# Kernel optimization log

Measured on AMD Instinct MI355X. Metric: run time of the kernel, lower is better.

## Reference

```python
import jax, jax.numpy as jnp
import numpy as np

N = 50000      # nodes
E = 800000     # edges (before self loops)
F_IN = 256     # input features
C = 64         # out_channels per head
H = 4          # heads
NC = 3         # num_class


def setup_inputs() -> dict:
    key = jax.random.key(0)
    ks = jax.random.split(key, 11)
    s = 0.1
    return {
        "x": jax.random.normal(ks[0], (N, F_IN), jnp.float32),
        "edge_index": jax.random.randint(ks[1], (2, E), 0, N, dtype=jnp.int64),
        # conv1: in=F_IN -> H*C, concat
        "W1": jax.random.normal(ks[2], (H * C, F_IN), jnp.float32) * s,
        "as1": jax.random.normal(ks[3], (H, C), jnp.float32) * s,
        "ad1": jax.random.normal(ks[4], (H, C), jnp.float32) * s,
        "b1": jnp.zeros((H * C,), jnp.float32),
        # conv2: in=H*C -> H*C, concat
        "W2": jax.random.normal(ks[5], (H * C, H * C), jnp.float32) * s,
        "as2": jax.random.normal(ks[6], (H, C), jnp.float32) * s,
        "ad2": jax.random.normal(ks[7], (H, C), jnp.float32) * s,
        "b2": jnp.zeros((H * C,), jnp.float32),
        # conv3: in=H*C -> NC, heads averaged (concat=False)
        "W3": jax.random.normal(ks[8], (H * NC, H * C), jnp.float32) * s,
        "as3": jax.random.normal(ks[9], (H, NC), jnp.float32) * s,
        "ad3": jax.random.normal(ks[10], (H, NC), jnp.float32) * s,
        "b3": jnp.zeros((NC,), jnp.float32),
    }


def _gat_conv(x, src, dst, W, a_src, a_dst, b, concat):
    # x: [N,F]; src/dst: [E'] (self loops included); W: [H*C, F]; a_*: [H,C]
    n = x.shape[0]
    h_, c_ = a_src.shape
    h = (x @ W.T).reshape(n, h_, c_)                       # [N,H,C]
    alpha_src = (h * a_src[None]).sum(-1)                  # [N,H]
    alpha_dst = (h * a_dst[None]).sum(-1)                  # [N,H]
    e = jax.nn.leaky_relu(alpha_src[src] + alpha_dst[dst], 0.2)  # [E',H]
    # segment softmax over destination-node neighborhoods
    m = jax.ops.segment_max(e, dst, num_segments=n)        # [N,H]
    ex = jnp.exp(e - m[dst])
    den = jax.ops.segment_sum(ex, dst, num_segments=n)     # [N,H]
    alpha = ex / den[dst]                                  # [E',H]
    out = jax.ops.segment_sum(h[src] * alpha[:, :, None], dst, num_segments=n)  # [N,H,C]
    if concat:
        return out.reshape(n, h_ * c_) + b
    return out.mean(axis=1) + b


def reference(x, edge_index, W1, as1, ad1, b1, W2, as2, ad2, b2, W3, as3, ad3, b3):
    n = x.shape[0]
    loop = jnp.arange(n, dtype=edge_index.dtype)
    src = jnp.concatenate([edge_index[0], loop])  # add_self_loops=True
    dst = jnp.concatenate([edge_index[1], loop])
    x = jax.nn.elu(_gat_conv(x, src, dst, W1, as1, ad1, b1, True))
    x = jax.nn.elu(_gat_conv(x, src, dst, W2, as2, ad2, b2, True))
    x = jax.nn.elu(_gat_conv(x, src, dst, W3, as3, ad3, b3, False))
    return x
```

## Files before the change

kernel.cpp:

```cpp
#include <hip/hip_runtime.h>
#include <hip/hip_fp16.h>
#include <cstdint>
#include <cstddef>

#define NNODES 50000
#define NEDGES 800000
#define E2 (NEDGES + NNODES)
#define HC 256

typedef __attribute__((ext_vector_type(8))) short short8v;
typedef __attribute__((ext_vector_type(4))) float f32x4;
typedef const __attribute__((address_space(1))) void* gas_t;
typedef __attribute__((address_space(3))) void* las_t;


__global__ void zero_int(int* __restrict__ p, int n) {
    int i = blockIdx.x * 256 + threadIdx.x;
    if (i < n) p[i] = 0;
}

__global__ void count_deg(const int* __restrict__ ei, int* __restrict__ deg) {
    int i = blockIdx.x * 256 + threadIdx.x;
    if (i >= E2) return;
    int d = (i < NEDGES) ? ei[NEDGES + i] : (i - NEDGES);
    atomicAdd(&deg[d], 1);
}

__global__ void scan1(const int* __restrict__ deg, int* __restrict__ rp, int* __restrict__ bs) {
    __shared__ int s[256];
    int t = threadIdx.x, i = blockIdx.x * 256 + t;
    int v = (i < NNODES) ? deg[i] : 0;
    s[t] = v;
    __syncthreads();
    for (int o = 1; o < 256; o <<= 1) {
        int add = (t >= o) ? s[t - o] : 0;
        __syncthreads();
        s[t] += add;
        __syncthreads();
    }
    if (i < NNODES) rp[i] = s[t] - v;
    if (t == 255) bs[blockIdx.x] = s[255];
}

__global__ void scan2(int* __restrict__ bs, int nb) {
    __shared__ int s[256];
    int t = threadIdx.x;
    int v = (t < nb) ? bs[t] : 0;
    s[t] = v;
    __syncthreads();
    for (int o = 1; o < 256; o <<= 1) {
        int add = (t >= o) ? s[t - o] : 0;
        __syncthreads();
        s[t] += add;
        __syncthreads();
    }
    bs[t] = s[t] - v;
}

__global__ void scan3(int* __restrict__ rp, const int* __restrict__ bs, int* __restrict__ cnt) {
    int i = blockIdx.x * 256 + threadIdx.x;
    if (i < NNODES) {
        int v = rp[i] + bs[blockIdx.x];
        rp[i] = v;
        cnt[i] = v;
    }
    if (i == 0) rp[NNODES] = E2;
}

__global__ void fill_csr(const int* __restrict__ ei, int* __restrict__ cnt, int* __restrict__ csr) {
    int i = blockIdx.x * 256 + threadIdx.x;
    if (i >= E2) return;
    int s, d;
    if (i < NEDGES) { s = ei[i]; d = ei[NEDGES + i]; }
    else            { s = d = i - NEDGES; }
    int pos = atomicAdd(&cnt[d], 1);
    csr[pos] = s;
}


__device__ __forceinline__ unsigned short f2bf(float f) {
    uint32_t u = __float_as_uint(f);
    uint32_t r = (u + 0x7FFFu + ((u >> 16) & 1u)) >> 16;
    return (unsigned short)r;
}
__device__ __forceinline__ float bf2f(unsigned short h) {
    return __uint_as_float(((uint32_t)h) << 16);
}

__global__ void split_bf16(const float* __restrict__ in, unsigned short* __restrict__ hi,
                           unsigned short* __restrict__ lo, int n4) {
    int i = blockIdx.x * 256 + threadIdx.x;
    if (i >= n4) return;
    float4 v = ((const float4*)in)[i];
    unsigned short h0 = f2bf(v.x), h1 = f2bf(v.y), h2 = f2bf(v.z), h3 = f2bf(v.w);
    unsigned short l0 = f2bf(v.x - bf2f(h0));
    unsigned short l1 = f2bf(v.y - bf2f(h1));
    unsigned short l2 = f2bf(v.z - bf2f(h2));
    unsigned short l3 = f2bf(v.w - bf2f(h3));
    uint2 hp, lp;
    hp.x = (uint32_t)h0 | ((uint32_t)h1 << 16);
    hp.y = (uint32_t)h2 | ((uint32_t)h3 << 16);
    lp.x = (uint32_t)l0 | ((uint32_t)l1 << 16);
    lp.y = (uint32_t)l2 | ((uint32_t)l3 << 16);
    *(uint2*)(hi + 4 * (size_t)i) = hp;
    *(uint2*)(lo + 4 * (size_t)i) = lp;
}


__global__ __launch_bounds__(256, 2) void gemm_mfma(
    const unsigned short* __restrict__ Ah, const unsigned short* __restrict__ Al,
    const unsigned short* __restrict__ Wh, const unsigned short* __restrict__ Wl,
    _Float16* __restrict__ out16, int M) {
    __shared__ unsigned short sAh[128][32], sAl[128][32], sWh[128][32], sWl[128][32];
    const int t = threadIdx.x;
    const int m0 = blockIdx.x * 128, n0 = blockIdx.y * 128;
    const int lane = t & 63, w = t >> 6;
    const int wr = w >> 1, wc = w & 1;
    const int fr = lane & 15, fg = lane >> 4;

    const int u0 = (w * 2) * 64 + lane, u1 = (w * 2 + 1) * 64 + lane;
    const int row0 = u0 >> 2, cb0 = (u0 & 3) * 8;
    const int row1 = u1 >> 2, cb1 = (u1 & 3) * 8;
    int gra0 = m0 + row0; gra0 = gra0 < M ? gra0 : M - 1;
    int gra1 = m0 + row1; gra1 = gra1 < M ? gra1 : M - 1;
    const int grw0 = n0 + row0, grw1 = n0 + row1;
    unsigned short* lA0 = &sAh[(w * 2) * 16][0];
    unsigned short* lA1 = &sAh[(w * 2 + 1) * 16][0];
    unsigned short* lB0 = &sAl[(w * 2) * 16][0];
    unsigned short* lB1 = &sAl[(w * 2 + 1) * 16][0];
    unsigned short* lC0 = &sWh[(w * 2) * 16][0];
    unsigned short* lC1 = &sWh[(w * 2 + 1) * 16][0];
    unsigned short* lD0 = &sWl[(w * 2) * 16][0];
    unsigned short* lD1 = &sWl[(w * 2 + 1) * 16][0];

    f32x4 acc[4][4];
#pragma unroll
    for (int mi = 0; mi < 4; mi++)
#pragma unroll
        for (int ni = 0; ni < 4; ni++) acc[mi][ni] = (f32x4){0.f, 0.f, 0.f, 0.f};

    for (int kc = 0; kc < 256; kc += 32) {
        __builtin_amdgcn_global_load_lds((gas_t)(Ah + (size_t)gra0 * HC + kc + cb0), (las_t)lA0, 16, 0, 0);
        __builtin_amdgcn_global_load_lds((gas_t)(Ah + (size_t)gra1 * HC + kc + cb1), (las_t)lA1, 16, 0, 0);
        __builtin_amdgcn_global_load_lds((gas_t)(Al + (size_t)gra0 * HC + kc + cb0), (las_t)lB0, 16, 0, 0);
        __builtin_amdgcn_global_load_lds((gas_t)(Al + (size_t)gra1 * HC + kc + cb1), (las_t)lB1, 16, 0, 0);
        __builtin_amdgcn_global_load_lds((gas_t)(Wh + (size_t)grw0 * HC + kc + cb0), (las_t)lC0, 16, 0, 0);
        __builtin_amdgcn_global_load_lds((gas_t)(Wh + (size_t)grw1 * HC + kc + cb1), (las_t)lC1, 16, 0, 0);
        __builtin_amdgcn_global_load_lds((gas_t)(Wl + (size_t)grw0 * HC + kc + cb0), (las_t)lD0, 16, 0, 0);
        __builtin_amdgcn_global_load_lds((gas_t)(Wl + (size_t)grw1 * HC + kc + cb1), (las_t)lD1, 16, 0, 0);
        __syncthreads();

        short8v ah[4], al[4], bh[4], bl[4];
#pragma unroll
        for (int i = 0; i < 4; i++) {
            ah[i] = *(const short8v*)&sAh[wr * 64 + i * 16 + fr][fg * 8];
            al[i] = *(const short8v*)&sAl[wr * 64 + i * 16 + fr][fg * 8];
            bh[i] = *(const short8v*)&sWh[wc * 64 + i * 16 + fr][fg * 8];
            bl[i] = *(const short8v*)&sWl[wc * 64 + i * 16 + fr][fg * 8];
        }
#pragma unroll
        for (int mi = 0; mi < 4; mi++)
#pragma unroll
            for (int ni = 0; ni < 4; ni++) {
                acc[mi][ni] = __builtin_amdgcn_mfma_f32_16x16x32_bf16(ah[mi], bh[ni], acc[mi][ni], 0, 0, 0);
                acc[mi][ni] = __builtin_amdgcn_mfma_f32_16x16x32_bf16(ah[mi], bl[ni], acc[mi][ni], 0, 0, 0);
                acc[mi][ni] = __builtin_amdgcn_mfma_f32_16x16x32_bf16(al[mi], bh[ni], acc[mi][ni], 0, 0, 0);
            }
        __syncthreads();
    }

#pragma unroll
    for (int mi = 0; mi < 4; mi++) {
#pragma unroll
        for (int r = 0; r < 4; r++) {
            int gr = m0 + wr * 64 + mi * 16 + fg * 4 + r;
            if (gr < M) {
#pragma unroll
                for (int ni = 0; ni < 4; ni++) {
                    out16[(size_t)gr * HC + n0 + wc * 64 + ni * 16 + fr] = (_Float16)acc[mi][ni][r];
                }
            }
        }
    }
}


__global__ void alpha_hc(const _Float16* __restrict__ h16, const float* __restrict__ a_s,
                         const float* __restrict__ a_d, float* __restrict__ asrc,
                         float* __restrict__ adst) {
    int n = blockIdx.x;
    int t = threadIdx.x;
    float v = (float)h16[(size_t)n * HC + t];
    float ps = v * a_s[t];
    float pd = v * a_d[t];
    for (int o = 32; o > 0; o >>= 1) {
        ps += __shfl_xor(ps, o);
        pd += __shfl_xor(pd, o);
    }
    if ((t & 63) == 0) {
        int w = t >> 6;
        asrc[n * 4 + w] = ps;
        adst[n * 4 + w] = pd;
    }
}


#define CHUNK 512

__global__ void aggregate_hc(const _Float16* __restrict__ h16, const float* __restrict__ asrc,
                             const float* __restrict__ adst, const int* __restrict__ rp,
                             const int* __restrict__ csr, const float* __restrict__ bias,
                             float* __restrict__ y, unsigned short* __restrict__ yh,
                             unsigned short* __restrict__ yl, int flags) {
    __shared__ int   sIdx[CHUNK];
    __shared__ float sE4[CHUNK][4];
    __shared__ float sM[4][4], sS[4][4];
    __shared__ float sRed[4][32][9];
    int n = blockIdx.x;
    int t = threadIdx.x;
    int r0 = rp[n], deg = rp[n + 1] - r0;

    if (deg <= CHUNK) {
        for (int j = t; j < deg; j += 256) sIdx[j] = csr[r0 + j];
        __syncthreads();

        int hA = t & 3, jj = t >> 2;
        float adh = adst[n * 4 + hA];
        float pm = -1e30f;
        for (int j = jj; j < deg; j += 64) {
            int s = sIdx[j];
            float e = asrc[s * 4 + hA] + adh;
            e = e > 0.f ? e : 0.2f * e;
            sE4[j][hA] = e;
            pm = fmaxf(pm, e);
        }
#pragma unroll
        for (int o = 4; o <= 32; o <<= 1) pm = fmaxf(pm, __shfl_xor(pm, o));
        if ((t & 63) < 4) sM[t >> 6][t & 3] = pm;
        __syncthreads();

        float mh = fmaxf(fmaxf(sM[0][hA], sM[1][hA]), fmaxf(sM[2][hA], sM[3][hA]));
        float ps = 0.f;
        for (int j = jj; j < deg; j += 64) {
            float ex = __expf(sE4[j][hA] - mh);
            sE4[j][hA] = ex;
            ps += ex;
        }
#pragma unroll
        for (int o = 4; o <= 32; o <<= 1) ps += __shfl_xor(ps, o);
        if ((t & 63) < 4) sS[t >> 6][t & 3] = ps;
        __syncthreads();

        int G = t >> 5, q = t & 31, hh = q >> 3;
        float a[8];
#pragma unroll
        for (int i = 0; i < 8; i++) a[i] = 0.f;
#pragma unroll 2
        for (int j = G; j < deg; j += 8) {
            int s = sIdx[j];
            float aw = sE4[j][hh];
            uint4 raw = *(const uint4*)(h16 + (size_t)s * HC + 8 * q);
            const _Float16* hv = reinterpret_cast<const _Float16*>(&raw);
#pragma unroll
            for (int i = 0; i < 8; i++) a[i] = fmaf((float)hv[i], aw, a[i]);
        }
#pragma unroll
        for (int i = 0; i < 8; i++) a[i] += __shfl_xor(a[i], 32);
        int wv = t >> 6, l = t & 63;
        if (l < 32) {
#pragma unroll
            for (int i = 0; i < 8; i++) sRed[wv][l][i] = a[i];
        }
        __syncthreads();

        int c = t;
        float val = sRed[0][c >> 3][c & 7] + sRed[1][c >> 3][c & 7]
                  + sRed[2][c >> 3][c & 7] + sRed[3][c >> 3][c & 7];
        int ch = c >> 6;
        float ssum = sS[0][ch] + sS[1][ch] + sS[2][ch] + sS[3][ch];
        float outv = val / ssum + bias[c];
        outv = outv > 0.f ? outv : expm1f(outv);
        size_t off = (size_t)n * HC + c;
        if (flags & 1) y[off] = outv;
        if (flags & 2) {
            unsigned short hi = f2bf(outv);
            yh[off] = hi;
            yl[off] = f2bf(outv - bf2f(hi));
        }
    } else {
        int w = t >> 6, l = t & 63;
        float ad = adst[n * 4 + w];
        int hoff = (w << 6) + l;
        const _Float16* hp = h16 + hoff;
        float m = -1e30f;
        for (int j = l; j < deg; j += 64) {
            int s = csr[r0 + j];
            float e = asrc[s * 4 + w] + ad;
            e = e > 0.f ? e : 0.2f * e;
            m = fmaxf(m, e);
        }
#pragma unroll
        for (int o = 32; o > 0; o >>= 1) m = fmaxf(m, __shfl_xor(m, o));
        float acc = 0.f, ssum = 0.f;
        for (int j = 0; j < deg; j++) {
            int s = csr[r0 + j];
            float e = asrc[s * 4 + w] + ad;
            e = e > 0.f ? e : 0.2f * e;
            float aa = __expf(e - m);
            ssum += aa;
            acc = fmaf(aa, (float)hp[(size_t)s * HC], acc);
        }
        float outv = acc / ssum + bias[hoff];
        outv = outv > 0.f ? outv : expm1f(outv);
        size_t off = (size_t)n * HC + hoff;
        if (flags & 1) y[off] = outv;
        if (flags & 2) {
            unsigned short hi = f2bf(outv);
            yh[off] = hi;
            yl[off] = f2bf(outv - bf2f(hi));
        }
    }
}


__global__ void gemm_small(const float* __restrict__ Y, const float* __restrict__ W3,
                           float* __restrict__ h3) {
    int idx = blockIdx.x * 256 + threadIdx.x;
    if (idx >= NNODES * 12) return;
    int n = idx / 12, o = idx - n * 12;
    const float4* xr = (const float4*)(Y + (size_t)n * HC);
    const float4* wr = (const float4*)(W3 + o * HC);
    float acc = 0.f;
#pragma unroll 8
    for (int k = 0; k < 64; k++) {
        float4 a = xr[k], b = wr[k];
        acc += a.x * b.x + a.y * b.y + a.z * b.z + a.w * b.w;
    }
    h3[idx] = acc;
}

__global__ void alpha3(const float* __restrict__ h3, const float* __restrict__ a_s,
                       const float* __restrict__ a_d, float* __restrict__ asrc,
                       float* __restrict__ adst) {
    int n = blockIdx.x * 256 + threadIdx.x;
    if (n >= NNODES) return;
    const float* hr = h3 + (size_t)n * 12;
    float s[4], d[4];
#pragma unroll
    for (int hh = 0; hh < 4; hh++) {
        s[hh] = hr[hh * 3] * a_s[hh * 3] + hr[hh * 3 + 1] * a_s[hh * 3 + 1] + hr[hh * 3 + 2] * a_s[hh * 3 + 2];
        d[hh] = hr[hh * 3] * a_d[hh * 3] + hr[hh * 3 + 1] * a_d[hh * 3 + 1] + hr[hh * 3 + 2] * a_d[hh * 3 + 2];
    }
    *(float4*)(asrc + n * 4) = make_float4(s[0], s[1], s[2], s[3]);
    *(float4*)(adst + n * 4) = make_float4(d[0], d[1], d[2], d[3]);
}

__global__ void aggregate3(const float* __restrict__ h3, const float* __restrict__ asrc,
                           const float* __restrict__ adst, const int* __restrict__ rp,
                           const int* __restrict__ csr, const float* __restrict__ b3,
                           float* __restrict__ out) {
    int n = blockIdx.x * 4 + (threadIdx.x >> 6);
    int l = threadIdx.x & 63;
    if (n >= NNODES) return;
    int r0 = rp[n], deg = rp[n + 1] - r0;
    float4 ad = *(const float4*)(adst + n * 4);

    float m0 = -1e30f, m1 = -1e30f, m2 = -1e30f, m3 = -1e30f;
    for (int j = l; j < deg; j += 64) {
        int s = csr[r0 + j];
        float4 a4 = *(const float4*)(asrc + s * 4);
        float e0 = a4.x + ad.x, e1 = a4.y + ad.y, e2 = a4.z + ad.z, e3 = a4.w + ad.w;
        e0 = e0 > 0.f ? e0 : 0.2f * e0;
        e1 = e1 > 0.f ? e1 : 0.2f * e1;
        e2 = e2 > 0.f ? e2 : 0.2f * e2;
        e3 = e3 > 0.f ? e3 : 0.2f * e3;
        m0 = fmaxf(m0, e0); m1 = fmaxf(m1, e1); m2 = fmaxf(m2, e2); m3 = fmaxf(m3, e3);
    }
    for (int o = 32; o > 0; o >>= 1) {
        m0 = fmaxf(m0, __shfl_xor(m0, o));
        m1 = fmaxf(m1, __shfl_xor(m1, o));
        m2 = fmaxf(m2, __shfl_xor(m2, o));
        m3 = fmaxf(m3, __shfl_xor(m3, o));
    }

    float acc[12];
#pragma unroll
    for (int k = 0; k < 12; k++) acc[k] = 0.f;
    float s0 = 0.f, s1 = 0.f, s2 = 0.f, s3 = 0.f;
    for (int j = l; j < deg; j += 64) {
        int s = csr[r0 + j];
        float4 a4 = *(const float4*)(asrc + s * 4);
        float e0 = a4.x + ad.x, e1 = a4.y + ad.y, e2 = a4.z + ad.z, e3 = a4.w + ad.w;
        e0 = e0 > 0.f ? e0 : 0.2f * e0;
        e1 = e1 > 0.f ? e1 : 0.2f * e1;
        e2 = e2 > 0.f ? e2 : 0.2f * e2;
        e3 = e3 > 0.f ? e3 : 0.2f * e3;
        float w0 = __expf(e0 - m0), w1 = __expf(e1 - m1), w2 = __expf(e2 - m2), w3 = __expf(e3 - m3);
        s0 += w0; s1 += w1; s2 += w2; s3 += w3;
        const float* hr = h3 + (size_t)s * 12;
#pragma unroll
        for (int c = 0; c < 3; c++) {
            acc[c]     += w0 * hr[c];
            acc[3 + c] += w1 * hr[3 + c];
            acc[6 + c] += w2 * hr[6 + c];
            acc[9 + c] += w3 * hr[9 + c];
        }
    }
    for (int o = 32; o > 0; o >>= 1) {
#pragma unroll
        for (int k = 0; k < 12; k++) acc[k] += __shfl_xor(acc[k], o);
        s0 += __shfl_xor(s0, o);
        s1 += __shfl_xor(s1, o);
        s2 += __shfl_xor(s2, o);
        s3 += __shfl_xor(s3, o);
    }
    if (l < 3) {
        float v = 0.25f * (acc[l] / s0 + acc[3 + l] / s1 + acc[6 + l] / s2 + acc[9 + l] / s3) + b3[l];
        v = v > 0.f ? v : expm1f(v);
        out[(size_t)n * 3 + l] = v;
    }
}


extern "C" void kernel_launch(void* const* d_in, const int* in_sizes, int n_in,
                              void* d_out, int out_size, void* d_ws, size_t ws_size,
                              hipStream_t stream) {
    (void)in_sizes; (void)n_in; (void)out_size; (void)ws_size;
    const float* x   = (const float*)d_in[0];
    const int*   ei  = (const int*)d_in[1];
    const float* W1  = (const float*)d_in[2];
    const float* as1 = (const float*)d_in[3];
    const float* ad1 = (const float*)d_in[4];
    const float* b1  = (const float*)d_in[5];
    const float* W2  = (const float*)d_in[6];
    const float* as2 = (const float*)d_in[7];
    const float* ad2 = (const float*)d_in[8];
    const float* b2  = (const float*)d_in[9];
    const float* W3  = (const float*)d_in[10];
    const float* as3 = (const float*)d_in[11];
    const float* ad3 = (const float*)d_in[12];
    const float* b3  = (const float*)d_in[13];
    float* out = (float*)d_out;

    uint8_t* p = (uint8_t*)d_ws;
    auto alloc = [&](size_t bytes) -> void* {
        void* r = (void*)p;
        p += (bytes + 255) & ~(size_t)255;
        return r;
    };
    float* bufY = (float*)alloc((size_t)NNODES * HC * 4);
    float* h3   = (float*)alloc((size_t)NNODES * 12 * 4);
    float* asrc = (float*)alloc((size_t)NNODES * 4 * 4);
    float* adst = (float*)alloc((size_t)NNODES * 4 * 4);
    int* deg    = (int*)alloc((size_t)NNODES * 4);
    int* rp     = (int*)alloc((size_t)(NNODES + 1) * 4);
    int* cnt    = (int*)alloc((size_t)NNODES * 4);
    int* csr    = (int*)alloc((size_t)E2 * 4);
    int* bsums  = (int*)alloc(256 * 4);
    unsigned short* xh  = (unsigned short*)alloc((size_t)NNODES * HC * 2);
    unsigned short* xl  = (unsigned short*)alloc((size_t)NNODES * HC * 2);
    unsigned short* w1h = (unsigned short*)alloc((size_t)HC * HC * 2);
    unsigned short* w1l = (unsigned short*)alloc((size_t)HC * HC * 2);
    unsigned short* w2h = (unsigned short*)alloc((size_t)HC * HC * 2);
    unsigned short* w2l = (unsigned short*)alloc((size_t)HC * HC * 2);
    _Float16* h16 = (_Float16*)alloc((size_t)NNODES * HC * 2);

    const int NB_N = (NNODES + 255) / 256;
    const int NB_E = (E2 + 255) / 256;
    const int N4_A = NNODES * HC / 4;
    const int N4_W = HC * HC / 4;

    zero_int<<<NB_N, 256, 0, stream>>>(deg, NNODES);
    count_deg<<<NB_E, 256, 0, stream>>>(ei, deg);
    scan1<<<NB_N, 256, 0, stream>>>(deg, rp, bsums);
    scan2<<<1, 256, 0, stream>>>(bsums, NB_N);
    scan3<<<NB_N, 256, 0, stream>>>(rp, bsums, cnt);
    fill_csr<<<NB_E, 256, 0, stream>>>(ei, cnt, csr);

    dim3 ggrid((NNODES + 127) / 128, 2);

    split_bf16<<<(N4_W + 255) / 256, 256, 0, stream>>>(W1, w1h, w1l, N4_W);
    split_bf16<<<(N4_A + 255) / 256, 256, 0, stream>>>(x, xh, xl, N4_A);
    gemm_mfma<<<ggrid, 256, 0, stream>>>(xh, xl, w1h, w1l, h16, NNODES);
    alpha_hc<<<NNODES, 256, 0, stream>>>(h16, as1, ad1, asrc, adst);
    aggregate_hc<<<NNODES, 256, 0, stream>>>(h16, asrc, adst, rp, csr, b1, bufY, xh, xl, 2);

    split_bf16<<<(N4_W + 255) / 256, 256, 0, stream>>>(W2, w2h, w2l, N4_W);
    gemm_mfma<<<ggrid, 256, 0, stream>>>(xh, xl, w2h, w2l, h16, NNODES);
    alpha_hc<<<NNODES, 256, 0, stream>>>(h16, as2, ad2, asrc, adst);
    aggregate_hc<<<NNODES, 256, 0, stream>>>(h16, asrc, adst, rp, csr, b2, bufY, xh, xl, 1);

    gemm_small<<<(NNODES * 12 + 255) / 256, 256, 0, stream>>>(bufY, W3, h3);
    alpha3<<<NB_N, 256, 0, stream>>>(h3, as3, ad3, asrc, adst);
    aggregate3<<<(NNODES + 3) / 4, 256, 0, stream>>>(h3, asrc, adst, rp, csr, b3, out);
}
```

Measured before the change: 664.4 us.

## Double-buffer GEMM LDS tiles and pack four nodes per alpha block

The MFMA GEMM now uses two LDS buffers so the global-to-LDS load of the next K tile is issued before computing the current one, with one barrier per iteration. This is meant to hide load latency behind the MFMAs, at the cost of doubling LDS per block, which may limit occupancy. The alpha kernel now handles four nodes per block with one wave per node, vectorised half and float4 loads, and 16-lane reductions per head. This cuts the launched block count and the number of scalar loads.

```diff
diff --git a/kernel.cpp b/kernel.cpp
--- a/kernel.cpp
+++ b/kernel.cpp
@@ -111,7 +111,7 @@
     const unsigned short* __restrict__ Ah, const unsigned short* __restrict__ Al,
     const unsigned short* __restrict__ Wh, const unsigned short* __restrict__ Wl,
     _Float16* __restrict__ out16, int M) {
-    __shared__ unsigned short sAh[128][32], sAl[128][32], sWh[128][32], sWl[128][32];
+    __shared__ unsigned short sAh[2][128][32], sAl[2][128][32], sWh[2][128][32], sWl[2][128][32];
     const int t = threadIdx.x;
     const int m0 = blockIdx.x * 128, n0 = blockIdx.y * 128;
     const int lane = t & 63, w = t >> 6;
@@ -124,14 +124,17 @@
     int gra0 = m0 + row0; gra0 = gra0 < M ? gra0 : M - 1;
     int gra1 = m0 + row1; gra1 = gra1 < M ? gra1 : M - 1;
     const int grw0 = n0 + row0, grw1 = n0 + row1;
-    unsigned short* lA0 = &sAh[(w * 2) * 16][0];
-    unsigned short* lA1 = &sAh[(w * 2 + 1) * 16][0];
-    unsigned short* lB0 = &sAl[(w * 2) * 16][0];
-    unsigned short* lB1 = &sAl[(w * 2 + 1) * 16][0];
-    unsigned short* lC0 = &sWh[(w * 2) * 16][0];
-    unsigned short* lC1 = &sWh[(w * 2 + 1) * 16][0];
-    unsigned short* lD0 = &sWl[(w * 2) * 16][0];
-    unsigned short* lD1 = &sWl[(w * 2 + 1) * 16][0];
+
+    auto stage = [&](int b, int kc) {
+        __builtin_amdgcn_global_load_lds((gas_t)(Ah + (size_t)gra0 * HC + kc + cb0), (las_t)&sAh[b][row0][cb0], 16, 0, 0);
+        __builtin_amdgcn_global_load_lds((gas_t)(Ah + (size_t)gra1 * HC + kc + cb1), (las_t)&sAh[b][row1][cb1], 16, 0, 0);
+        __builtin_amdgcn_global_load_lds((gas_t)(Al + (size_t)gra0 * HC + kc + cb0), (las_t)&sAl[b][row0][cb0], 16, 0, 0);
+        __builtin_amdgcn_global_load_lds((gas_t)(Al + (size_t)gra1 * HC + kc + cb1), (las_t)&sAl[b][row1][cb1], 16, 0, 0);
+        __builtin_amdgcn_global_load_lds((gas_t)(Wh + (size_t)grw0 * HC + kc + cb0), (las_t)&sWh[b][row0][cb0], 16, 0, 0);
+        __builtin_amdgcn_global_load_lds((gas_t)(Wh + (size_t)grw1 * HC + kc + cb1), (las_t)&sWh[b][row1][cb1], 16, 0, 0);
+        __builtin_amdgcn_global_load_lds((gas_t)(Wl + (size_t)grw0 * HC + kc + cb0), (las_t)&sWl[b][row0][cb0], 16, 0, 0);
+        __builtin_amdgcn_global_load_lds((gas_t)(Wl + (size_t)grw1 * HC + kc + cb1), (las_t)&sWl[b][row1][cb1], 16, 0, 0);
+    };
 
     f32x4 acc[4][4];
 #pragma unroll
@@ -139,24 +142,14 @@
 #pragma unroll
         for (int ni = 0; ni < 4; ni++) acc[mi][ni] = (f32x4){0.f, 0.f, 0.f, 0.f};
 
-    for (int kc = 0; kc < 256; kc += 32) {
-        __builtin_amdgcn_global_load_lds((gas_t)(Ah + (size_t)gra0 * HC + kc + cb0), (las_t)lA0, 16, 0, 0);
-        __builtin_amdgcn_global_load_lds((gas_t)(Ah + (size_t)gra1 * HC + kc + cb1), (las_t)lA1, 16, 0, 0);
-        __builtin_amdgcn_global_load_lds((gas_t)(Al + (size_t)gra0 * HC + kc + cb0), (las_t)lB0, 16, 0, 0);
-        __builtin_amdgcn_global_load_lds((gas_t)(Al + (size_t)gra1 * HC + kc + cb1), (las_t)lB1, 16, 0, 0);
-        __builtin_amdgcn_global_load_lds((gas_t)(Wh + (size_t)grw0 * HC + kc + cb0), (las_t)lC0, 16, 0, 0);
-        __builtin_amdgcn_global_load_lds((gas_t)(Wh + (size_t)grw1 * HC + kc + cb1), (las_t)lC1, 16, 0, 0);
-        __builtin_amdgcn_global_load_lds((gas_t)(Wl + (size_t)grw0 * HC + kc + cb0), (las_t)lD0, 16, 0, 0);
-        __builtin_amdgcn_global_load_lds((gas_t)(Wl + (size_t)grw1 * HC + kc + cb1), (las_t)lD1, 16, 0, 0);
-        __syncthreads();
-
+    auto compute = [&](int b) {
         short8v ah[4], al[4], bh[4], bl[4];
 #pragma unroll
         for (int i = 0; i < 4; i++) {
-            ah[i] = *(const short8v*)&sAh[wr * 64 + i * 16 + fr][fg * 8];
-            al[i] = *(const short8v*)&sAl[wr * 64 + i * 16 + fr][fg * 8];
-            bh[i] = *(const short8v*)&sWh[wc * 64 + i * 16 + fr][fg * 8];
-            bl[i] = *(const short8v*)&sWl[wc * 64 + i * 16 + fr][fg * 8];
+            ah[i] = *(const short8v*)&sAh[b][wr * 64 + i * 16 + fr][fg * 8];
+            al[i] = *(const short8v*)&sAl[b][wr * 64 + i * 16 + fr][fg * 8];
+            bh[i] = *(const short8v*)&sWh[b][wc * 64 + i * 16 + fr][fg * 8];
+            bl[i] = *(const short8v*)&sWl[b][wc * 64 + i * 16 + fr][fg * 8];
         }
 #pragma unroll
         for (int mi = 0; mi < 4; mi++)
@@ -166,8 +159,17 @@
                 acc[mi][ni] = __builtin_amdgcn_mfma_f32_16x16x32_bf16(ah[mi], bl[ni], acc[mi][ni], 0, 0, 0);
                 acc[mi][ni] = __builtin_amdgcn_mfma_f32_16x16x32_bf16(al[mi], bh[ni], acc[mi][ni], 0, 0, 0);
             }
-        __syncthreads();
-    }
+    };
+
+    stage(0, 0);
+    __syncthreads();
+#pragma unroll
+    for (int kt = 0; kt < 7; kt++) {
+        stage((kt + 1) & 1, (kt + 1) * 32);
+        compute(kt & 1);
+        __syncthreads();
+    }
+    compute(1);
 
 #pragma unroll
     for (int mi = 0; mi < 4; mi++) {
@@ -188,19 +190,26 @@
 __global__ void alpha_hc(const _Float16* __restrict__ h16, const float* __restrict__ a_s,
                          const float* __restrict__ a_d, float* __restrict__ asrc,
                          float* __restrict__ adst) {
-    int n = blockIdx.x;
-    int t = threadIdx.x;
-    float v = (float)h16[(size_t)n * HC + t];
-    float ps = v * a_s[t];
-    float pd = v * a_d[t];
-    for (int o = 32; o > 0; o >>= 1) {
+    int n = blockIdx.x * 4 + (threadIdx.x >> 6);
+    int lane = threadIdx.x & 63;
+    uint2 raw = *(const uint2*)(h16 + (size_t)n * HC + lane * 4);
+    __half2 p0 = *(__half2*)&raw.x;
+    __half2 p1 = *(__half2*)&raw.y;
+    float h0 = __low2float(p0), h1 = __high2float(p0);
+    float h2 = __low2float(p1), h3 = __high2float(p1);
+    float4 s4 = *(const float4*)(a_s + lane * 4);
+    float4 d4 = *(const float4*)(a_d + lane * 4);
+    float ps = h0 * s4.x + h1 * s4.y + h2 * s4.z + h3 * s4.w;
+    float pd = h0 * d4.x + h1 * d4.y + h2 * d4.z + h3 * d4.w;
+#pragma unroll
+    for (int o = 1; o < 16; o <<= 1) {
         ps += __shfl_xor(ps, o);
         pd += __shfl_xor(pd, o);
     }
-    if ((t & 63) == 0) {
-        int w = t >> 6;
-        asrc[n * 4 + w] = ps;
-        adst[n * 4 + w] = pd;
+    if ((lane & 15) == 0) {
+        int hh = lane >> 4;
+        asrc[n * 4 + hh] = ps;
+        adst[n * 4 + hh] = pd;
     }
 }
 
@@ -482,12 +491,12 @@
     split_bf16<<<(N4_W + 255) / 256, 256, 0, stream>>>(W1, w1h, w1l, N4_W);
     split_bf16<<<(N4_A + 255) / 256, 256, 0, stream>>>(x, xh, xl, N4_A);
     gemm_mfma<<<ggrid, 256, 0, stream>>>(xh, xl, w1h, w1l, h16, NNODES);
-    alpha_hc<<<NNODES, 256, 0, stream>>>(h16, as1, ad1, asrc, adst);
+    alpha_hc<<<NNODES / 4, 256, 0, stream>>>(h16, as1, ad1, asrc, adst);
     aggregate_hc<<<NNODES, 256, 0, stream>>>(h16, asrc, adst, rp, csr, b1, bufY, xh, xl, 2);
 
     split_bf16<<<(N4_W + 255) / 256, 256, 0, stream>>>(W2, w2h, w2l, N4_W);
     gemm_mfma<<<ggrid, 256, 0, stream>>>(xh, xl, w2h, w2l, h16, NNODES);
-    alpha_hc<<<NNODES, 256, 0, stream>>>(h16, as2, ad2, asrc, adst);
+    alpha_hc<<<NNODES / 4, 256, 0, stream>>>(h16, as2, ad2, asrc, adst);
     aggregate_hc<<<NNODES, 256, 0, stream>>>(h16, asrc, adst, rp, csr, b2, bufY, xh, xl, 1);
 
     gemm_small<<<(NNODES * 12 + 255) / 256, 256, 0, stream>>>(bufY, W3, h3);
```

Result: faster. 640.2 us (-3.6%).
